# Kernel optimization log

Hardware: AMD Instinct MI355X
Metric: run time of the kernel (lower is better)

Reference implementation:

```python
import jax, jax.numpy as jnp
import numpy as np

B, N, K = 32, 1024, 20          # graphs, points per graph, kNN neighbors
EMB = 1024                       # emb_dims
OUT = 7                          # out_channels
WS1, ST1, G1 = 52, 20, 7         # linear1 STFT-KAN: window, stride, gridsize
WS2, ST2, G2 = 197, 7, 6         # linear2 STFT-KAN
NW1 = (128 - WS1) // ST1 + 1     # 4 windows over 128-dim features
NW2 = (2 * EMB - WS2) // ST2 + 1 # 265 windows over 2048-dim features


def _window(kind, M):
    n = jnp.arange(M, dtype=jnp.float32)
    if kind == 'bartlett':
        return 1.0 - jnp.abs(2.0 * n / M - 1.0)        # periodic bartlett (torch default)
    return 0.5 * (1.0 - jnp.cos(2.0 * jnp.pi * n / M)) # periodic hann


def _stft_kan(x, coeffs, bias, gridsize, ws, stride, wtype):
    """x: [B, D]; coeffs: [2, outdim, nw, ws, gridsize]; returns [B, outdim]."""
    D = x.shape[1]
    nw = (D - ws) // stride + 1
    idx = jnp.arange(nw)[:, None] * stride + jnp.arange(ws)[None, :]  # [nw, ws]
    xw = x[:, idx] * _window(wtype, ws)                               # [B, nw, ws]
    kk = jnp.arange(1, gridsize + 1, dtype=x.dtype)
    ang = xw[..., None] * kk                                          # [B, nw, ws, g]
    y = jnp.einsum('bnwg,onwg->bo', jnp.cos(ang), coeffs[0])
    y = y + jnp.einsum('bnwg,onwg->bo', jnp.sin(ang), coeffs[1])
    return y + bias


def setup_inputs() -> dict:
    key = jax.random.key(0)
    ks = jax.random.split(key, 8)
    pos = jax.random.normal(ks[0], (B * N, 3), jnp.float32)
    batch = jnp.repeat(jnp.arange(B, dtype=jnp.int32), N)  # sorted, equal-size graphs
    # EdgeConv MLP([6,64,128]): Linear+BN+ReLU, then plain Linear
    W1 = jax.random.normal(ks[1], (6, 64), jnp.float32) * 0.3
    b1 = jnp.zeros((64,), jnp.float32)
    gamma1 = jnp.ones((64,), jnp.float32)
    beta1 = jnp.zeros((64,), jnp.float32)
    W2 = jax.random.normal(ks[2], (64, 128), jnp.float32) * 0.1
    b2 = jnp.zeros((128,), jnp.float32)
    # STFT-KAN 1 (smooth init: coeffs damped by k^2)
    k1 = np.arange(1, G1 + 1, dtype=np.float32)
    c1 = jax.random.normal(ks[3], (2, EMB, NW1, WS1, G1), jnp.float32) / (np.sqrt(NW1 * WS1) * (k1 ** 2))
    bi1 = jnp.zeros((EMB,), jnp.float32)
    # STFT-KAN 2 (non-smooth init)
    c2 = jax.random.normal(ks[4], (2, OUT, NW2, WS2, G2), jnp.float32) / (np.sqrt(NW2 * WS2) * np.sqrt(G2))
    bi2 = jnp.zeros((OUT,), jnp.float32)
    return {"pos": pos, "batch": batch, "W1": W1, "b1": b1, "gamma1": gamma1,
            "beta1": beta1, "W2": W2, "b2": b2, "c1": c1, "bi1": bi1, "c2": c2, "bi2": bi2}


def reference(pos, batch, W1, b1, gamma1, beta1, W2, b2, c1, bi1, c2, bi2):
    p = pos.reshape(B, N, 3)
    # dynamic kNN graph per batch element (exclude self)
    sq = jnp.sum(p * p, axis=-1)                                    # [B, N]
    d2 = sq[:, :, None] + sq[:, None, :] - 2.0 * jnp.einsum('bnd,bmd->bnm', p, p)
    d2 = d2 + jnp.eye(N, dtype=p.dtype) * 1e10
    _, idx = jax.lax.top_k(-d2, K)                                  # [B, N, K]
    pj = jax.vmap(lambda pts, ids: pts[ids])(p, idx)                # [B, N, K, 3]
    pi = jnp.broadcast_to(p[:, :, None, :], (B, N, K, 3))
    e = jnp.concatenate([pi, pj - pi], axis=-1)                     # [B, N, K, 6]
    # edge MLP: Linear -> BN -> ReLU -> Linear
    h = e @ W1 + b1
    mu = h.mean((0, 1, 2))
    var = h.var((0, 1, 2))
    h = gamma1 * (h - mu) * jax.lax.rsqrt(var + 1e-5) + beta1
    h = jax.nn.relu(h)
    h = h @ W2 + b2                                                 # [B, N, K, 128]
    x1 = h.max(axis=2).reshape(B * N, 128)                          # max aggregation over neighbors
    x = _stft_kan(x1, c1, bi1, G1, WS1, ST1, 'bartlett')            # [B*N, EMB]
    xg = x.reshape(B, N, EMB)
    xcat = jnp.concatenate([xg.max(axis=1), xg.mean(axis=1)], axis=-1)  # global max/mean pool
    return _stft_kan(xcat, c2, bi2, G2, WS2, ST2, 'hann')           # [B, OUT]
```

## Files before the change

### kernel.cpp

```cpp
#include <hip/hip_runtime.h>
#include <cstdint>

typedef _Float16 half8 __attribute__((ext_vector_type(8)));
typedef float f32x4 __attribute__((ext_vector_type(4)));

__device__ __forceinline__ void gload16(const void* g, void* l) {
  __builtin_amdgcn_global_load_lds(
      (const __attribute__((address_space(1))) void*)g,
      (__attribute__((address_space(3))) void*)l, 16, 0, 0);
}

__global__ __launch_bounds__(256) void knn_kernel(const float* __restrict__ pos,
                                                  int* __restrict__ nbr) {
  __shared__ float px[1024], py[1024], pz[1024], sq[1024];
  int tid = threadIdx.x;
  int b = blockIdx.x >> 8;
  const float* pg = pos + (size_t)b * 3072;
  for (int m = 0; m < 4; ++m) {
    int j = m * 256 + tid;
    float x = pg[3 * j], y = pg[3 * j + 1], z = pg[3 * j + 2];
    px[j] = x; py[j] = y; pz[j] = z; sq[j] = x * x + y * y + z * z;
  }
  __syncthreads();
  int wave = tid >> 6, lane = tid & 63;
  int n = (blockIdx.x & 255) * 4 + wave;
  float xi = px[n], yi = py[n], zi = pz[n], si = sq[n];
  float d[16];
#pragma unroll
  for (int i = 0; i < 16; ++i) {
    int j = i * 64 + lane;
    float dd = si + sq[j] - 2.0f * (xi * px[j] + yi * py[j] + zi * pz[j]);
    d[i] = (j == n) ? 1e30f : dd;
  }
  int outbase = (b * 1024 + n) * 20;
  for (int kk = 0; kk < 20; ++kk) {
    float lmin = d[0]; int lpos = 0;
#pragma unroll
    for (int i = 1; i < 16; ++i)
      if (d[i] < lmin) { lmin = d[i]; lpos = i; }
    float bv = lmin; int bi = lpos * 64 + lane;
#pragma unroll
    for (int off = 1; off < 64; off <<= 1) {
      float ov = __shfl_xor(bv, off);
      int   oi = __shfl_xor(bi, off);
      if (ov < bv || (ov == bv && oi < bi)) { bv = ov; bi = oi; }
    }
    if (lane == 0) nbr[outbase + kk] = b * 1024 + bi;
    if ((bi & 63) == lane) {
      int rp = bi >> 6;
#pragma unroll
      for (int i = 0; i < 16; ++i)
        if (i == rp) d[i] = 1e30f;
    }
  }
}

__global__ __launch_bounds__(256) void edge_stats_kernel(
    const float* __restrict__ pos, const int* __restrict__ nbr,
    const float* __restrict__ W1, const float* __restrict__ b1v,
    float* __restrict__ psum, float* __restrict__ psq) {
  __shared__ float els[256][6];
  __shared__ float w1s[384];
  __shared__ float b1s[64];
  __shared__ float red[8][64];
  int tid = threadIdx.x, bid = blockIdx.x;
  for (int f = tid; f < 384; f += 256) w1s[f] = W1[f];
  if (tid < 64) b1s[tid] = b1v[tid];
  int c = tid & 63, grp = tid >> 6;
  float s = 0.f, s2 = 0.f;
  for (int ch = 0; ch < 5; ++ch) {
    int E = bid * 1280 + ch * 256 + tid;
    int p = E / 20;
    int j = nbr[E];
    float pix = pos[3 * p], piy = pos[3 * p + 1], piz = pos[3 * p + 2];
    float e3 = pos[3 * j] - pix, e4 = pos[3 * j + 1] - piy, e5 = pos[3 * j + 2] - piz;
    __syncthreads();
    els[tid][0] = pix; els[tid][1] = piy; els[tid][2] = piz;
    els[tid][3] = e3;  els[tid][4] = e4;  els[tid][5] = e5;
    __syncthreads();
    for (int m = 0; m < 64; ++m) {
      int e = grp * 64 + m;
      float h = b1s[c];
#pragma unroll
      for (int d = 0; d < 6; ++d) h += els[e][d] * w1s[d * 64 + c];
      s += h; s2 += h * h;
    }
  }
  red[grp][c] = s;
  __syncthreads();
  red[4 + grp][c] = s2;
  __syncthreads();
  if (tid < 64) {
    float S = red[0][tid] + red[1][tid] + red[2][tid] + red[3][tid];
    float Q = red[4][tid] + red[5][tid] + red[6][tid] + red[7][tid];
    psum[bid * 64 + tid] = S;
    psq[bid * 64 + tid] = Q;
  }
}

__global__ void bn_finalize_kernel(const float* __restrict__ psum, const float* __restrict__ psq,
                                   const float* __restrict__ gamma, const float* __restrict__ beta,
                                   float* __restrict__ bns, float* __restrict__ bnh) {
  int c = threadIdx.x;
  float s = 0.f, q = 0.f;
  for (int b = 0; b < 512; ++b) { s += psum[b * 64 + c]; q += psq[b * 64 + c]; }
  const float inv = 1.0f / 655360.0f;
  float mu = s * inv;
  float var = q * inv - mu * mu;
  float sc = gamma[c] * rsqrtf(var + 1e-5f);
  bns[c] = sc;
  bnh[c] = beta[c] - mu * sc;
}

__global__ __launch_bounds__(256) void edge_mlp_kernel(
    const float* __restrict__ pos, const int* __restrict__ nbr,
    const float* __restrict__ W1, const float* __restrict__ b1v,
    const float* __restrict__ bns, const float* __restrict__ bnh,
    const float* __restrict__ W2, const float* __restrict__ b2v,
    float* __restrict__ x1) {
  __shared__ __align__(16) char elds[53248];
  _Float16* Ah = (_Float16*)(elds);
  _Float16* Al = (_Float16*)(elds + 10240);
  _Float16* Bh = (_Float16*)(elds + 20480);
  _Float16* Bl = (_Float16*)(elds + 36864);
  float* outb = (float*)elds;
  __shared__ float w1s[384];
  __shared__ float b1s[64], scs[64], shs[64];
  int tid = threadIdx.x, bid = blockIdx.x;
  for (int f = tid; f < 384; f += 256) w1s[f] = W1[f];
  if (tid < 64) { b1s[tid] = b1v[tid]; scs[tid] = bns[tid]; shs[tid] = bnh[tid]; }
#pragma unroll
  for (int i = 0; i < 32; ++i) {
    int flat = tid + 256 * i;
    int dd = flat >> 7, c = flat & 127;
    float v = W2[flat];
    _Float16 hi = (_Float16)v;
    _Float16 lo = (_Float16)(v - (float)hi);
    int byte = c * 128 + ((((dd >> 3) ^ (c & 7))) << 4) + (dd & 7) * 2;
    *(_Float16*)((char*)Bh + byte) = hi;
    *(_Float16*)((char*)Bl + byte) = lo;
  }
  __syncthreads();
#pragma unroll
  for (int m = 0; m < 20; ++m) {
    int flat = tid + 256 * m;
    int row = flat >> 6;
    int d = flat & 63;
    int j = nbr[bid * 80 + row];
    int P = bid * 4 + (row / 20);
    float pix = pos[3 * P], piy = pos[3 * P + 1], piz = pos[3 * P + 2];
    float e3 = pos[3 * j] - pix, e4 = pos[3 * j + 1] - piy, e5 = pos[3 * j + 2] - piz;
    float h = b1s[d];
    h += pix * w1s[d] + piy * w1s[64 + d] + piz * w1s[128 + d]
       + e3 * w1s[192 + d] + e4 * w1s[256 + d] + e5 * w1s[320 + d];
    h = scs[d] * h + shs[d];
    h = fmaxf(h, 0.f);
    _Float16 hi = (_Float16)h;
    _Float16 lo = (_Float16)(h - (float)hi);
    int byte = row * 128 + ((((d >> 3) ^ (row & 7))) << 4) + (d & 7) * 2;
    *(_Float16*)((char*)Ah + byte) = hi;
    *(_Float16*)((char*)Al + byte) = lo;
  }
  __syncthreads();
  int wave = tid >> 6, lane = tid & 63;
  int l15 = lane & 15, l4 = lane >> 4;
  f32x4 acc[5][2] = {};
#pragma unroll
  for (int ks = 0; ks < 2; ++ks) {
    int slotk = ks * 4 + l4;
    half8 bfh[2], bfl[2];
#pragma unroll
    for (int ci = 0; ci < 2; ++ci) {
      int col = (wave * 2 + ci) * 16 + l15;
      int byte = col * 128 + ((slotk ^ (col & 7)) << 4);
      bfh[ci] = *(const half8*)((char*)Bh + byte);
      bfl[ci] = *(const half8*)((char*)Bl + byte);
    }
#pragma unroll
    for (int rt = 0; rt < 5; ++rt) {
      int row = rt * 16 + l15;
      int byte = row * 128 + ((slotk ^ (row & 7)) << 4);
      half8 ah = *(const half8*)((char*)Ah + byte);
      half8 al = *(const half8*)((char*)Al + byte);
#pragma unroll
      for (int ci = 0; ci < 2; ++ci) {
        acc[rt][ci] = __builtin_amdgcn_mfma_f32_16x16x32_f16(ah, bfh[ci], acc[rt][ci], 0, 0, 0);
        acc[rt][ci] = __builtin_amdgcn_mfma_f32_16x16x32_f16(ah, bfl[ci], acc[rt][ci], 0, 0, 0);
        acc[rt][ci] = __builtin_amdgcn_mfma_f32_16x16x32_f16(al, bfh[ci], acc[rt][ci], 0, 0, 0);
      }
    }
  }
  __syncthreads();
#pragma unroll
  for (int rt = 0; rt < 5; ++rt)
#pragma unroll
    for (int ci = 0; ci < 2; ++ci) {
      int col = (wave * 2 + ci) * 16 + l15;
#pragma unroll
      for (int q = 0; q < 4; ++q) {
        int row = rt * 16 + l4 * 4 + q;
        outb[row * 129 + col] = acc[rt][ci][q];
      }
    }
  __syncthreads();
#pragma unroll
  for (int r = 0; r < 2; ++r) {
    int it = tid + 256 * r;
    int p = it >> 7, c = it & 127;
    float mx = -1e30f;
#pragma unroll
    for (int e = 0; e < 20; ++e) mx = fmaxf(mx, outb[(p * 20 + e) * 129 + c]);
    x1[((size_t)bid * 4 + p) * 128 + c] = mx + b2v[c];
  }
}

__global__ void kan1_tables_kernel(int* __restrict__ dimt, float* __restrict__ wkt) {
  int j = blockIdx.x * 256 + threadIdx.x;
  if (j >= 2944) return;
  if (j >= 2912) { dimt[j] = 0; wkt[j] = 0.0f; return; }
  int r = j % 1456;
  int n = r / 364, r2 = r % 364;
  int w = r2 / 7, g = r2 % 7;
  dimt[j] = n * 20 + w;
  float bart = 1.0f - fabsf(2.0f * (float)w / 52.0f - 1.0f);
  wkt[j] = bart * (float)(g + 1);
}

__global__ void c1_to_f16_kernel(const float* __restrict__ c1, _Float16* __restrict__ Cf) {
  int L = blockIdx.x * 256 + threadIdx.x;
  if (L >= 1024 * 2944) return;
  int o = L / 2944, j = L % 2944;
  float v = 0.0f;
  if (j < 2912) {
    int t = j / 1456, r = j % 1456;
    v = c1[(size_t)(t * 1024 + o) * 1456 + r];
  }
  Cf[L] = (_Float16)v;
}

__global__ __launch_bounds__(512, 2) void kan1_gemm_kernel(
    const float* __restrict__ x1, const _Float16* __restrict__ Cf,
    const int* __restrict__ dimt, const float* __restrict__ wkt,
    float* __restrict__ pmax, float* __restrict__ psump) {
  __shared__ __align__(16) _Float16 Asm[2][128 * 64];
  __shared__ __align__(16) _Float16 Bsm[2][256 * 64];
  __shared__ int   tdim[2][64];
  __shared__ float twk[2][64];
  int tid = threadIdx.x;
  int bm = blockIdx.x, bn = blockIdx.y;
  int m0 = bm << 7, n0 = bn << 8;
  int wave = tid >> 6, lane = tid & 63;
  int wr = wave >> 2, wc = wave & 3;
  int l15 = lane & 15, l4 = lane >> 4;

  auto stageB = [&](int t, int nb) {
    int j0 = t << 6;
#pragma unroll
    for (int i = 0; i < 4; ++i) {
      int idx = i * 512 + tid;
      int col = idx >> 3, slot = idx & 7;
      int sslot = slot ^ (col & 7);
      gload16(Cf + (size_t)(n0 + col) * 2944 + j0 + sslot * 8,
              (char*)Bsm[nb] + idx * 16);
    }
  };
  auto agen = [&](int t, int nb) {
    const int* td = tdim[t & 1];
    const float* tw = twk[t & 1];
    int j0 = t << 6;
#pragma unroll
    for (int rep = 0; rep < 2; ++rep) {
      int slot = tid + rep * 512;
      int r = slot >> 3, s = slot & 7;
      const float* xrow = x1 + (size_t)(m0 + r) * 128;
      int d0 = td[s * 8], d7 = td[s * 8 + 7];
      float x0 = xrow[d0], x7 = xrow[d7];
      half8 av;
#pragma unroll
      for (int e = 0; e < 8; ++e) {
        int jj = s * 8 + e;
        float xv = (td[jj] == d0) ? x0 : x7;
        float ph = (j0 + jj >= 1456) ? 1.57079632679489662f : 0.0f;
        av[e] = (_Float16)__cosf(xv * tw[jj] - ph);
      }
      *(half8*)((char*)Asm[nb] + r * 128 + ((s ^ (r & 7)) << 4)) = av;
    }
  };

  if (tid < 64)                { tdim[0][tid]      = dimt[tid];            twk[0][tid]      = wkt[tid]; }
  else if (tid < 128)          { tdim[1][tid - 64] = dimt[tid];            twk[1][tid - 64] = wkt[tid]; }
  f32x4 acc[4][4] = {};
  __syncthreads();
  stageB(0, 0);
  agen(0, 0);
  __syncthreads();

  for (int t = 0; t < 46; ++t) {
    int cur = t & 1, nxt = cur ^ 1;
    if (t < 45) stageB(t + 1, nxt);
    half8 af[2][4], bf[2][4];
#pragma unroll
    for (int ksub = 0; ksub < 2; ++ksub) {
      int slotk = ksub * 4 + l4;
#pragma unroll
      for (int mi = 0; mi < 4; ++mi) {
        int row = wr * 64 + mi * 16 + l15;
        af[ksub][mi] = *(const half8*)((char*)Asm[cur] + row * 128 + ((slotk ^ (row & 7)) << 4));
      }
#pragma unroll
      for (int ni = 0; ni < 4; ++ni) {
        int col = wc * 64 + ni * 16 + l15;
        bf[ksub][ni] = *(const half8*)((char*)Bsm[cur] + col * 128 + ((slotk ^ (col & 7)) << 4));
      }
    }
    if (t < 45) agen(t + 1, nxt);
    if (t < 44 && tid < 64) {
      tdim[cur][tid] = dimt[(t + 2) * 64 + tid];
      twk[cur][tid]  = wkt[(t + 2) * 64 + tid];
    }
#pragma unroll
    for (int ksub = 0; ksub < 2; ++ksub)
#pragma unroll
      for (int mi = 0; mi < 4; ++mi)
#pragma unroll
        for (int ni = 0; ni < 4; ++ni)
          acc[mi][ni] = __builtin_amdgcn_mfma_f32_16x16x32_f16(af[ksub][mi], bf[ksub][ni], acc[mi][ni], 0, 0, 0);
    __syncthreads();
  }

  float* pooled = (float*)Asm;
#pragma unroll
  for (int ni = 0; ni < 4; ++ni) {
    float mx = -1e30f, sm = 0.f;
#pragma unroll
    for (int mi = 0; mi < 4; ++mi)
#pragma unroll
      for (int q = 0; q < 4; ++q) {
        float v = acc[mi][ni][q];
        mx = fmaxf(mx, v); sm += v;
      }
    mx = fmaxf(mx, __shfl_xor(mx, 16)); sm += __shfl_xor(sm, 16);
    mx = fmaxf(mx, __shfl_xor(mx, 32)); sm += __shfl_xor(sm, 32);
    if (l4 == 0) {
      int col = wc * 64 + ni * 16 + l15;
      pooled[(wr * 2 + 0) * 256 + col] = mx;
      pooled[(wr * 2 + 1) * 256 + col] = sm;
    }
  }
  __syncthreads();
  if (tid < 256) {
    float mx = fmaxf(pooled[tid], pooled[512 + tid]);
    float sm = pooled[256 + tid] + pooled[768 + tid];
    pmax[(size_t)bm * 1024 + n0 + tid] = mx;
    psump[(size_t)bm * 1024 + n0 + tid] = sm;
  }
}

__global__ void pool_reduce_kernel(const float* __restrict__ pmax, const float* __restrict__ psump,
                                   const float* __restrict__ bi1,
                                   float* __restrict__ gmax, float* __restrict__ gmean) {
  int gid = blockIdx.x * 256 + threadIdx.x;
  int b = gid >> 10, col = gid & 1023;
  float mx = -1e30f, sm = 0.f;
  for (int t = 0; t < 8; ++t) {
    mx = fmaxf(mx, pmax[(size_t)(b * 8 + t) * 1024 + col]);
    sm += psump[(size_t)(b * 8 + t) * 1024 + col];
  }
  float bias = bi1[col];
  gmax[gid] = mx + bias;
  gmean[gid] = sm * (1.0f / 1024.0f) + bias;
}

__global__ __launch_bounds__(256) void kan2_kernel(
    const float* __restrict__ gmax, const float* __restrict__ gmean,
    const float* __restrict__ c2, float* __restrict__ part) {
  __shared__ float xc[2048];
  __shared__ float hw[197];
  __shared__ float racc[7][256];
  int b = blockIdx.x, s = blockIdx.y, tid = threadIdx.x;
  for (int f = tid; f < 1024; f += 256) {
    xc[f] = gmax[b * 1024 + f];
    xc[1024 + f] = gmean[b * 1024 + f];
  }
  for (int f = tid; f < 197; f += 256)
    hw[f] = 0.5f * (1.0f - cosf(6.283185307179586f * (float)f / 197.0f));
  float acc[7] = {};
  __syncthreads();
  int qlo = (52205 * s) / 16, qhi = (52205 * (s + 1)) / 16;
  for (int q = qlo + tid; q < qhi; q += 256) {
    int n = q / 197;
    int w = q - n * 197;
    float xw = xc[n * 7 + w] * hw[w];
    float s1, c1v;
    __sincosf(xw, &s1, &c1v);
    float ckv[6], skv[6];
    {
      float ck = c1v, sk = s1;
#pragma unroll
      for (int g = 0; g < 6; ++g) {
        ckv[g] = ck; skv[g] = sk;
        float cn = ck * c1v - sk * s1;
        sk = sk * c1v + ck * s1;
        ck = cn;
      }
    }
    int base = q * 6;
#pragma unroll
    for (int o = 0; o < 7; ++o) {
      const float* pc = c2 + (size_t)o * 313230 + base;
      const float* ps = c2 + (size_t)(o + 7) * 313230 + base;
      float sc = 0.f, ss = 0.f;
#pragma unroll
      for (int g = 0; g < 6; ++g) { sc += ckv[g] * pc[g]; ss += skv[g] * ps[g]; }
      acc[o] += sc + ss;
    }
  }
#pragma unroll
  for (int o = 0; o < 7; ++o) racc[o][tid] = acc[o];
  __syncthreads();
  for (int st = 128; st >= 1; st >>= 1) {
    if (tid < st)
#pragma unroll
      for (int o = 0; o < 7; ++o) racc[o][tid] += racc[o][tid + st];
    __syncthreads();
  }
  if (tid < 7) part[(b * 16 + s) * 7 + tid] = racc[tid][0];
}

__global__ void kan2_reduce_kernel(const float* __restrict__ part, const float* __restrict__ bi2,
                                   float* __restrict__ out) {
  int i = threadIdx.x;
  if (i >= 224) return;
  int b = i / 7, o = i % 7;
  float s = 0.f;
  for (int t = 0; t < 16; ++t) s += part[(b * 16 + t) * 7 + o];
  out[b * 7 + o] = s + bi2[o];
}

extern "C" void kernel_launch(void* const* d_in, const int* in_sizes, int n_in,
                              void* d_out, int out_size, void* d_ws, size_t ws_size,
                              hipStream_t stream) {
  const float* pos    = (const float*)d_in[0];
  const float* W1     = (const float*)d_in[2];
  const float* b1     = (const float*)d_in[3];
  const float* gamma1 = (const float*)d_in[4];
  const float* beta1  = (const float*)d_in[5];
  const float* W2     = (const float*)d_in[6];
  const float* b2     = (const float*)d_in[7];
  const float* c1     = (const float*)d_in[8];
  const float* bi1    = (const float*)d_in[9];
  const float* c2     = (const float*)d_in[10];
  const float* bi2    = (const float*)d_in[11];
  float* out = (float*)d_out;
  char* ws = (char*)d_ws;

  int*      nbr   = (int*)     (ws + 0);
  float*    x1    = (float*)   (ws + 2621440);
  _Float16* Cf    = (_Float16*)(ws + 19398656);
  int*      dimt  = (int*)     (ws + 25427968);
  float*    wkt   = (float*)   (ws + 25439744);
  float*    psum  = (float*)   (ws + 25451520);
  float*    psq   = (float*)   (ws + 25582592);
  float*    bns   = (float*)   (ws + 25713664);
  float*    bnh   = (float*)   (ws + 25713920);
  float*    pmax  = (float*)   (ws + 25714176);
  float*    psump = (float*)   (ws + 26762752);
  float*    gmax  = (float*)   (ws + 27811328);
  float*    gmean = (float*)   (ws + 27942400);
  float*    part  = (float*)   (ws + 28073472);
  if (ws_size < 28087808) return;

  knn_kernel<<<8192, 256, 0, stream>>>(pos, nbr);
  kan1_tables_kernel<<<12, 256, 0, stream>>>(dimt, wkt);
  c1_to_f16_kernel<<<11776, 256, 0, stream>>>(c1, Cf);
  edge_stats_kernel<<<512, 256, 0, stream>>>(pos, nbr, W1, b1, psum, psq);
  bn_finalize_kernel<<<1, 64, 0, stream>>>(psum, psq, gamma1, beta1, bns, bnh);
  edge_mlp_kernel<<<8192, 256, 0, stream>>>(pos, nbr, W1, b1, bns, bnh, W2, b2, x1);
  kan1_gemm_kernel<<<dim3(256, 4), 512, 0, stream>>>(x1, Cf, dimt, wkt, pmax, psump);
  pool_reduce_kernel<<<128, 256, 0, stream>>>(pmax, psump, bi1, gmax, gmean);
  kan2_kernel<<<dim3(32, 16), 256, 0, stream>>>(gmax, gmean, c2, part);
  kan2_reduce_kernel<<<1, 256, 0, stream>>>(part, bi2, out);
}
```

Measured before the change: 601.5 us.

## Generate KAN1 cos/sin harmonics via Chebyshev recurrence with padded per-window K layout

Reorders the KAN1 GEMM K dimension so each 8-element slot holds the 7 harmonics of one (window position, feature chunk, cos/sin) tuple, padded to 8. One sincos plus a Chebyshev recurrence then produces all harmonics, replacing seven transcendental calls per slot. The 128x112 slice of x1 is staged into LDS once and the index/weight lookup tables and their kernel are removed. The cost is a larger K (3328 vs 2944, 52 vs 46 iterations) with zero padding, more LDS use, and recurrence error in fp16.

Result: no change. 592.9 us (-1.4%).

```diff
diff --git a/kernel.cpp b/kernel.cpp
--- a/kernel.cpp
+++ b/kernel.cpp
@@ -214,38 +214,25 @@
   }
 }
 
-__global__ void kan1_tables_kernel(int* __restrict__ dimt, float* __restrict__ wkt) {
-  int j = blockIdx.x * 256 + threadIdx.x;
-  if (j >= 2944) return;
-  if (j >= 2912) { dimt[j] = 0; wkt[j] = 0.0f; return; }
-  int r = j % 1456;
-  int n = r / 364, r2 = r % 364;
-  int w = r2 / 7, g = r2 % 7;
-  dimt[j] = n * 20 + w;
-  float bart = 1.0f - fabsf(2.0f * (float)w / 52.0f - 1.0f);
-  wkt[j] = bart * (float)(g + 1);
-}
-
 __global__ void c1_to_f16_kernel(const float* __restrict__ c1, _Float16* __restrict__ Cf) {
   int L = blockIdx.x * 256 + threadIdx.x;
-  if (L >= 1024 * 2944) return;
-  int o = L / 2944, j = L % 2944;
+  if (L >= 1024 * 3328) return;
+  int o = L / 3328, rem = L % 3328;
+  int w = rem >> 6, idx = rem & 63;
+  int s = idx >> 3, e = idx & 7;
+  int phase = s >> 2, n = s & 3;
   float v = 0.0f;
-  if (j < 2912) {
-    int t = j / 1456, r = j % 1456;
-    v = c1[(size_t)(t * 1024 + o) * 1456 + r];
-  }
+  if (e < 7)
+    v = c1[((((size_t)phase * 1024 + o) * 4 + n) * 52 + w) * 7 + e];
   Cf[L] = (_Float16)v;
 }
 
 __global__ __launch_bounds__(512, 2) void kan1_gemm_kernel(
     const float* __restrict__ x1, const _Float16* __restrict__ Cf,
-    const int* __restrict__ dimt, const float* __restrict__ wkt,
     float* __restrict__ pmax, float* __restrict__ psump) {
+  __shared__ __align__(16) float xs[128 * 112];
   __shared__ __align__(16) _Float16 Asm[2][128 * 64];
   __shared__ __align__(16) _Float16 Bsm[2][256 * 64];
-  __shared__ int   tdim[2][64];
-  __shared__ float twk[2][64];
   int tid = threadIdx.x;
   int bm = blockIdx.x, bn = blockIdx.y;
   int m0 = bm << 7, n0 = bn << 8;
@@ -260,44 +247,54 @@
       int idx = i * 512 + tid;
       int col = idx >> 3, slot = idx & 7;
       int sslot = slot ^ (col & 7);
-      gload16(Cf + (size_t)(n0 + col) * 2944 + j0 + sslot * 8,
+      gload16(Cf + (size_t)(n0 + col) * 3328 + j0 + sslot * 8,
               (char*)Bsm[nb] + idx * 16);
     }
   };
+  int sA = tid & 7;
+  int phA = sA >> 2, nA = sA & 3;
   auto agen = [&](int t, int nb) {
-    const int* td = tdim[t & 1];
-    const float* tw = twk[t & 1];
-    int j0 = t << 6;
+    float bart = 1.0f - fabsf((float)(2 * t) * (1.0f / 52.0f) - 1.0f);
+    int d = nA * 20 + t;
 #pragma unroll
     for (int rep = 0; rep < 2; ++rep) {
-      int slot = tid + rep * 512;
-      int r = slot >> 3, s = slot & 7;
-      const float* xrow = x1 + (size_t)(m0 + r) * 128;
-      int d0 = td[s * 8], d7 = td[s * 8 + 7];
-      float x0 = xrow[d0], x7 = xrow[d7];
+      int r = (tid >> 3) + rep * 64;
+      float th = xs[r * 112 + d] * bart;
+      float sn, cs;
+      __sincosf(th, &sn, &cs);
+      float c2 = 2.0f * cs;
+      float p0 = phA ? sn : cs;
+      float p1 = phA ? c2 * sn : c2 * cs - 1.0f;
       half8 av;
-#pragma unroll
-      for (int e = 0; e < 8; ++e) {
-        int jj = s * 8 + e;
-        float xv = (td[jj] == d0) ? x0 : x7;
-        float ph = (j0 + jj >= 1456) ? 1.57079632679489662f : 0.0f;
-        av[e] = (_Float16)__cosf(xv * tw[jj] - ph);
-      }
-      *(half8*)((char*)Asm[nb] + r * 128 + ((s ^ (r & 7)) << 4)) = av;
+      av[0] = (_Float16)p0; av[1] = (_Float16)p1;
+      float pm2 = p0, pm1 = p1;
+#pragma unroll
+      for (int g = 2; g < 7; ++g) {
+        float pg = c2 * pm1 - pm2;
+        av[g] = (_Float16)pg;
+        pm2 = pm1; pm1 = pg;
+      }
+      av[7] = (_Float16)0.0f;
+      *(half8*)((char*)Asm[nb] + r * 128 + ((sA ^ (r & 7)) << 4)) = av;
     }
   };
 
-  if (tid < 64)                { tdim[0][tid]      = dimt[tid];            twk[0][tid]      = wkt[tid]; }
-  else if (tid < 128)          { tdim[1][tid - 64] = dimt[tid];            twk[1][tid - 64] = wkt[tid]; }
+#pragma unroll
+  for (int i = 0; i < 7; ++i) {
+    int idx = i * 512 + tid;
+    int f = idx * 4;
+    int row = f / 112, col = f - row * 112;
+    gload16(x1 + (size_t)(m0 + row) * 128 + col, (char*)xs + idx * 16);
+  }
+  stageB(0, 0);
   f32x4 acc[4][4] = {};
   __syncthreads();
-  stageB(0, 0);
   agen(0, 0);
   __syncthreads();
 
-  for (int t = 0; t < 46; ++t) {
+  for (int t = 0; t < 52; ++t) {
     int cur = t & 1, nxt = cur ^ 1;
-    if (t < 45) stageB(t + 1, nxt);
+    if (t < 51) stageB(t + 1, nxt);
     half8 af[2][4], bf[2][4];
 #pragma unroll
     for (int ksub = 0; ksub < 2; ++ksub) {
@@ -313,11 +310,7 @@
         bf[ksub][ni] = *(const half8*)((char*)Bsm[cur] + col * 128 + ((slotk ^ (col & 7)) << 4));
       }
     }
-    if (t < 45) agen(t + 1, nxt);
-    if (t < 44 && tid < 64) {
-      tdim[cur][tid] = dimt[(t + 2) * 64 + tid];
-      twk[cur][tid]  = wkt[(t + 2) * 64 + tid];
-    }
+    if (t < 51) agen(t + 1, nxt);
 #pragma unroll
     for (int ksub = 0; ksub < 2; ++ksub)
 #pragma unroll
@@ -328,7 +321,7 @@
     __syncthreads();
   }
 
-  float* pooled = (float*)Asm;
+  float* pooled = (float*)xs;
 #pragma unroll
   for (int ni = 0; ni < 4; ++ni) {
     float mx = -1e30f, sm = 0.f;
@@ -457,26 +450,23 @@
   int*      nbr   = (int*)     (ws + 0);
   float*    x1    = (float*)   (ws + 2621440);
   _Float16* Cf    = (_Float16*)(ws + 19398656);
-  int*      dimt  = (int*)     (ws + 25427968);
-  float*    wkt   = (float*)   (ws + 25439744);
-  float*    psum  = (float*)   (ws + 25451520);
-  float*    psq   = (float*)   (ws + 25582592);
-  float*    bns   = (float*)   (ws + 25713664);
-  float*    bnh   = (float*)   (ws + 25713920);
-  float*    pmax  = (float*)   (ws + 25714176);
-  float*    psump = (float*)   (ws + 26762752);
-  float*    gmax  = (float*)   (ws + 27811328);
-  float*    gmean = (float*)   (ws + 27942400);
-  float*    part  = (float*)   (ws + 28073472);
-  if (ws_size < 28087808) return;
+  float*    psum  = (float*)   (ws + 26214400);
+  float*    psq   = (float*)   (ws + 26345472);
+  float*    bns   = (float*)   (ws + 26476544);
+  float*    bnh   = (float*)   (ws + 26476800);
+  float*    pmax  = (float*)   (ws + 26477056);
+  float*    psump = (float*)   (ws + 27525632);
+  float*    gmax  = (float*)   (ws + 28574208);
+  float*    gmean = (float*)   (ws + 28705280);
+  float*    part  = (float*)   (ws + 28836352);
+  if (ws_size < 28850688) return;
 
   knn_kernel<<<8192, 256, 0, stream>>>(pos, nbr);
-  kan1_tables_kernel<<<12, 256, 0, stream>>>(dimt, wkt);
-  c1_to_f16_kernel<<<11776, 256, 0, stream>>>(c1, Cf);
+  c1_to_f16_kernel<<<13312, 256, 0, stream>>>(c1, Cf);
   edge_stats_kernel<<<512, 256, 0, stream>>>(pos, nbr, W1, b1, psum, psq);
   bn_finalize_kernel<<<1, 64, 0, stream>>>(psum, psq, gamma1, beta1, bns, bnh);
   edge_mlp_kernel<<<8192, 256, 0, stream>>>(pos, nbr, W1, b1, bns, bnh, W2, b2, x1);
-  kan1_gemm_kernel<<<dim3(256, 4), 512, 0, stream>>>(x1, Cf, dimt, wkt, pmax, psump);
+  kan1_gemm_kernel<<<dim3(256, 4), 512, 0, stream>>>(x1, Cf, pmax, psump);
   pool_reduce_kernel<<<128, 256, 0, stream>>>(pmax, psump, bi1, gmax, gmean);
   kan2_kernel<<<dim3(32, 16), 256, 0, stream>>>(gmax, gmean, c2, part);
   kan2_reduce_kernel<<<1, 256, 0, stream>>>(part, bi2, out);
```
